# Optimization experiments

Measured on AMD Instinct MI355X. Metric: run time of the kernel, lower is better.

## Reference

```python
import jax, jax.numpy as jnp
import numpy as np

MODEL_DIM = 128
N_ATOMS = 2048
ATOM_SIZE = 512
N_SAMPLES = 2 ** 15
FACTOR = 1.0
TAU = 1.0
B, E = 8, 64


def _stack(x, w0, b0, w1, b1, w2, b2):
    # LinearOutputStack(model_dim, 2, out_channels=...): 2 hidden layers + output
    h = jax.nn.leaky_relu(x @ w0 + b0, 0.2)
    h = jax.nn.leaky_relu(h @ w1 + b1, 0.2)
    return h @ w2 + b2


def _fft_shift(a, shift):
    # a: [B, E, n], shift: [B, E, 1] (fractional shift in units of n samples * 0.5)
    n = a.shape[-1]
    shift_samples = shift * n * 0.5  # [B, E, 1]
    a = jnp.pad(a, ((0, 0), (0, 0), (0, n * 2)))
    spec = jnp.fft.rfft(a, axis=-1, norm='ortho')  # [B, E, n_coeffs] complex
    n_coeffs = spec.shape[-1]
    phase = (jnp.arange(n_coeffs) * 2j * jnp.pi) / n_coeffs  # [n_coeffs]
    spec = spec * jnp.exp(-phase[None, None, :] * shift_samples)
    samples = jnp.fft.irfft(spec, axis=-1, norm='ortho')
    return samples[..., :n]


def setup_inputs() -> dict:
    key = jax.random.key(0)
    ks = jax.random.split(key, 24)
    w = lambda k, i, o: (jax.random.normal(k, (i, o), jnp.float32) * 0.1)
    z = lambda o: jnp.zeros((o,), jnp.float32)
    return {
        'x': jax.random.normal(ks[0], (B, E, MODEL_DIM), jnp.float32),
        'times': jax.random.uniform(ks[1], (B, E, 1), jnp.float32),
        'gumbel_u': jax.random.uniform(ks[2], (B, E, N_ATOMS), jnp.float32),
        'atoms': jax.random.uniform(ks[3], (N_ATOMS, ATOM_SIZE), jnp.float32, -1.0, 1.0),
        'tw0': w(ks[4], MODEL_DIM, MODEL_DIM), 'tb0': z(MODEL_DIM),
        'tw1': w(ks[5], MODEL_DIM, MODEL_DIM), 'tb1': z(MODEL_DIM),
        'tw2': w(ks[6], MODEL_DIM, 1), 'tb2': z(1),
        'sw0': w(ks[7], MODEL_DIM, MODEL_DIM), 'sb0': z(MODEL_DIM),
        'sw1': w(ks[8], MODEL_DIM, MODEL_DIM), 'sb1': z(MODEL_DIM),
        'sw2': w(ks[9], MODEL_DIM, N_ATOMS), 'sb2': z(N_ATOMS),
        'aw0': w(ks[10], MODEL_DIM, MODEL_DIM), 'ab0': z(MODEL_DIM),
        'aw1': w(ks[11], MODEL_DIM, MODEL_DIM), 'ab1': z(MODEL_DIM),
        'aw2': w(ks[12], MODEL_DIM, 1), 'ab2': z(1),
    }


def reference(x, times, gumbel_u, atoms,
              tw0, tb0, tw1, tb1, tw2, tb2,
              sw0, sb0, sw1, sb1, sw2, sb2,
              aw0, ab0, aw1, ab1, aw2, ab2):
    time = jax.nn.sigmoid(_stack(x, tw0, tb0, tw1, tb1, tw2, tb2)) * FACTOR + times  # [B,E,1]
    amp = _stack(x, aw0, ab0, aw1, ab1, aw2, ab2) ** 2  # [B,E,1]
    logits = _stack(x, sw0, sb0, sw1, sb1, sw2, sb2)  # [B,E,N_ATOMS]

    # hard gumbel-softmax with straight-through estimator
    eps = 1e-10
    g = -jnp.log(-jnp.log(gumbel_u + eps) + eps)
    y_soft = jax.nn.softmax((logits + g) / TAU, axis=-1)
    y_hard = jax.nn.one_hot(jnp.argmax(y_soft, axis=-1), N_ATOMS, dtype=y_soft.dtype)
    sel = y_hard - jax.lax.stop_gradient(y_soft) + y_soft

    normed = atoms / (jnp.linalg.norm(atoms, axis=-1, keepdims=True) + 1e-8)
    a = (sel @ normed) * amp  # [B,E,ATOM_SIZE]
    a = jnp.pad(a, ((0, 0), (0, 0), (0, N_SAMPLES - ATOM_SIZE)))  # [B,E,N_SAMPLES]
    final = _fft_shift(a, time)
    return jnp.sum(final, axis=1, keepdims=True)  # [B,1,N_SAMPLES]
```

## Files before the change

kernel.cpp:

```cpp
#include <hip/hip_runtime.h>
#include <math.h>

#define MD 128
#define NA 2048
#define AS 512
#define NS 32768
#define NBE 512
#define W1 768
#define W2 1280
#define PI 3.14159265358979323846
#define KTH ((float)(PI / 98304.0))

__device__ __forceinline__ float lrelu(float v) { return v > 0.f ? v : 0.2f * v; }

__device__ __forceinline__ float p8_far(float tf, float4 A, float4 B, float4 C)
{
  float u  = tf - A.x;
  float th = u * KTH;
  float sn = __sinf(th);
  float cs = __cosf(th);
  float c  = cs * __builtin_amdgcn_rcpf(sn);
  float u2  = __builtin_fmaf(c, c, 1.f);
  float c2  = c + c;
  float u22 = u2 + u2;
  float a2  = c * u2;
  float a3  = (-1.f / 3.f) * __builtin_fmaf(c2, a2, u2 * u2);
  float a4  = 0.5f * __builtin_fmaf(-c, a3, u2 * a2);
  float s5  = __builtin_fmaf(c2, a4, a2 * a2);
  s5        = __builtin_fmaf(-u22, a3, s5);
  float a5  = -0.2f * s5;
  float s6  = __builtin_fmaf(c, a5, a2 * a3);
  s6        = __builtin_fmaf(-u2, a4, s6);
  float a6  = (-1.f / 3.f) * s6;
  float s7  = __builtin_fmaf(c2, a6, a3 * a3);
  s7        = __builtin_fmaf(-u22, a5, s7);
  s7        = __builtin_fmaf(2.f * a2, a4, s7);
  float a7  = (-1.f / 7.f) * s7;
  float s8  = __builtin_fmaf(c, a7, a3 * a4);
  s8        = __builtin_fmaf(-u2, a6, s8);
  s8        = __builtin_fmaf(a2, a5, s8);
  float a8  = -0.25f * s8;
  float y = c * A.w;
  y = __builtin_fmaf(-u2, B.x, y);
  y = __builtin_fmaf(a2, B.y, y);
  y = __builtin_fmaf(a3, B.z, y);
  y = __builtin_fmaf(a4, B.w, y);
  y = __builtin_fmaf(a5, C.x, y);
  y = __builtin_fmaf(a6, C.y, y);
  y = __builtin_fmaf(a7, C.z, y);
  y = __builtin_fmaf(a8, C.w, y);
  bool farq = (tf < A.y) || (tf >= A.z);
  return farq ? y : 0.f;
}

__global__ __launch_bounds__(128) void hidden_kernel(
    const float* __restrict__ x, const float* __restrict__ times,
    const float* __restrict__ tw0, const float* __restrict__ tb0,
    const float* __restrict__ tw1, const float* __restrict__ tb1,
    const float* __restrict__ tw2, const float* __restrict__ tb2,
    const float* __restrict__ sw0, const float* __restrict__ sb0,
    const float* __restrict__ sw1, const float* __restrict__ sb1,
    const float* __restrict__ aw0, const float* __restrict__ ab0,
    const float* __restrict__ aw1, const float* __restrict__ ab1,
    const float* __restrict__ aw2, const float* __restrict__ ab2,
    float* __restrict__ timev, float* __restrict__ ampv,
    float* __restrict__ h2sel, float* __restrict__ out)
{
  const int rg = blockIdx.x;
  const int stack = blockIdx.y;
  const int tid = threadIdx.x;

  {
    const int gtid = (stack * 256 + rg) * 128 + tid;
    if (gtid < (8 * NS) / 4)
      ((float4*)out)[gtid] = make_float4(0.f, 0.f, 0.f, 0.f);
  }

  __shared__ float xs[2][MD];
  __shared__ double dA[2][MD], dB[2][MD];
  __shared__ float fA[2][MD], fB[2][MD];

#pragma unroll
  for (int j = 0; j < 2; ++j) xs[j][tid] = x[(rg * 2 + j) * MD + tid];
  __syncthreads();

  if (stack == 0) {
    {
      double b = (double)tb0[tid];
      double s[2] = {b, b};
#pragma unroll 8
      for (int k = 0; k < MD; ++k) {
        double w = (double)tw0[k * MD + tid];
#pragma unroll
        for (int j = 0; j < 2; ++j) s[j] += (double)xs[j][k] * w;
      }
#pragma unroll
      for (int j = 0; j < 2; ++j) dA[j][tid] = s[j] > 0.0 ? s[j] : 0.2 * s[j];
      __syncthreads();
    }
    {
      double b = (double)tb1[tid];
      double s[2] = {b, b};
#pragma unroll 8
      for (int k = 0; k < MD; ++k) {
        double w = (double)tw1[k * MD + tid];
#pragma unroll
        for (int j = 0; j < 2; ++j) s[j] += dA[j][k] * w;
      }
#pragma unroll
      for (int j = 0; j < 2; ++j) dB[j][tid] = s[j] > 0.0 ? s[j] : 0.2 * s[j];
      __syncthreads();
    }
    {
      double w2 = (double)tw2[tid];
#pragma unroll
      for (int j = 0; j < 2; ++j) dA[j][tid] = dB[j][tid] * w2;
      __syncthreads();
      for (int off = 64; off > 0; off >>= 1) {
        if (tid < off) {
#pragma unroll
          for (int j = 0; j < 2; ++j) dA[j][tid] += dA[j][tid + off];
        }
        __syncthreads();
      }
      if (tid == 0) {
#pragma unroll
        for (int j = 0; j < 2; ++j) {
          double tval = dA[j][0] + (double)tb2[0];
          double sg = 1.0 / (1.0 + exp(-tval));
          float tf = (float)sg;
          timev[rg * 2 + j] = tf * 1.0f + times[rg * 2 + j];
        }
      }
    }
  } else if (stack == 1) {
    {
      float b = ab0[tid];
      float s[2] = {b, b};
#pragma unroll 8
      for (int k = 0; k < MD; ++k) {
        float w = aw0[k * MD + tid];
#pragma unroll
        for (int j = 0; j < 2; ++j) s[j] += xs[j][k] * w;
      }
#pragma unroll
      for (int j = 0; j < 2; ++j) fA[j][tid] = lrelu(s[j]);
      __syncthreads();
    }
    {
      float b = ab1[tid];
      float s[2] = {b, b};
#pragma unroll 8
      for (int k = 0; k < MD; ++k) {
        float w = aw1[k * MD + tid];
#pragma unroll
        for (int j = 0; j < 2; ++j) s[j] += fA[j][k] * w;
      }
#pragma unroll
      for (int j = 0; j < 2; ++j) fB[j][tid] = lrelu(s[j]);
      __syncthreads();
    }
    {
      float w2 = aw2[tid];
#pragma unroll
      for (int j = 0; j < 2; ++j) fA[j][tid] = fB[j][tid] * w2;
      __syncthreads();
      for (int off = 64; off > 0; off >>= 1) {
        if (tid < off) {
#pragma unroll
          for (int j = 0; j < 2; ++j) fA[j][tid] += fA[j][tid + off];
        }
        __syncthreads();
      }
      if (tid == 0) {
#pragma unroll
        for (int j = 0; j < 2; ++j) {
          float av = fA[j][0] + ab2[0];
          ampv[rg * 2 + j] = av * av;
        }
      }
    }
  } else {
    {
      float b = sb0[tid];
      float s[2] = {b, b};
#pragma unroll 8
      for (int k = 0; k < MD; ++k) {
        float w = sw0[k * MD + tid];
#pragma unroll
        for (int j = 0; j < 2; ++j) s[j] += xs[j][k] * w;
      }
#pragma unroll
      for (int j = 0; j < 2; ++j) fA[j][tid] = lrelu(s[j]);
      __syncthreads();
    }
    {
      float b = sb1[tid];
      float s[2] = {b, b};
#pragma unroll 8
      for (int k = 0; k < MD; ++k) {
        float w = sw1[k * MD + tid];
#pragma unroll
        for (int j = 0; j < 2; ++j) s[j] += fA[j][k] * w;
      }
#pragma unroll
      for (int j = 0; j < 2; ++j)
        h2sel[(rg * 2 + j) * MD + tid] = lrelu(s[j]);
    }
  }
}

__global__ __launch_bounds__(128) void logits_kernel(
    const float* __restrict__ h2sel, const float* __restrict__ gu,
    const float* __restrict__ sw2, const float* __restrict__ sb2,
    float2* __restrict__ partials)
{
  const int ot = blockIdx.x;
  const int beg = blockIdx.y;
  const int tid = threadIdx.x;
  const int o = ot * 128 + tid;
  const int wave = tid >> 6, lane = tid & 63;

  __shared__ float h2s[4][MD];
  __shared__ float wv[2][4];
  __shared__ int wi[2][4];

#pragma unroll
  for (int j = 0; j < 4; ++j) h2s[j][tid] = h2sel[(beg * 4 + j) * MD + tid];
  __syncthreads();

  float b = sb2[o];
  float acc[4] = {b, b, b, b};
#pragma unroll 16
  for (int k = 0; k < MD; ++k) {
    float w = sw2[k * NA + o];
#pragma unroll
    for (int j = 0; j < 4; ++j) acc[j] = fmaf(h2s[j][k], w, acc[j]);
  }

#pragma unroll
  for (int j = 0; j < 4; ++j) {
    float u = gu[(beg * 4 + j) * NA + o];
    float g = -__logf(-__logf(u + 1e-10f) + 1e-10f);
    float v = acc[j] + g;
    int idx = o;
    for (int off = 32; off > 0; off >>= 1) {
      float ov = __shfl_xor(v, off);
      int oi = __shfl_xor(idx, off);
      if (ov > v || (ov == v && oi < idx)) { v = ov; idx = oi; }
    }
    if (lane == 0) { wv[wave][j] = v; wi[wave][j] = idx; }
  }
  __syncthreads();
  if (tid == 0) {
#pragma unroll
    for (int j = 0; j < 4; ++j) {
      float v0 = wv[0][j], v1 = wv[1][j];
      int i0 = wi[0][j], i1 = wi[1][j];
      bool take1 = (v1 > v0) || (v1 == v0 && i1 < i0);
      float bv = take1 ? v1 : v0;
      int bi = take1 ? i1 : i0;
      partials[(beg * 4 + j) * 16 + ot] = make_float2(bv, __int_as_float(bi));
    }
  }
}

__global__ __launch_bounds__(128) void finalize_kernel(
    const float2* __restrict__ partials, const float* __restrict__ timev,
    const float* __restrict__ ampv, const float* __restrict__ atoms,
    float* __restrict__ G, int* __restrict__ m0s, float* __restrict__ fracs,
    float4* __restrict__ params, float4* __restrict__ mom2)
{
  const int be = blockIdx.x;
  const int tid = threadIdx.x;
  __shared__ float red[128];
  __shared__ float m_red[128][13];
  __shared__ float sc_coef, sc_inv;
  __shared__ int sc_idx;

  if (tid < 64) {
    float v = -3.4e38f;
    int idx = 0x7fffffff;
    if (tid < 16) {
      float2 p = partials[be * 16 + tid];
      v = p.x;
      idx = __float_as_int(p.y);
    }
    for (int off = 8; off > 0; off >>= 1) {
      float ov = __shfl_xor(v, off);
      int oi = __shfl_xor(idx, off);
      if (ov > v || (ov == v && oi < idx)) { v = ov; idx = oi; }
    }
    if (tid == 0) sc_idx = idx;
  }
  __syncthreads();
  const int idx = sc_idx;

  const float4 a4 = ((const float4*)(atoms + (size_t)idx * AS))[tid];

  {
    float ss = a4.x * a4.x + a4.y * a4.y + a4.z * a4.z + a4.w * a4.w;
    red[tid] = ss;
    __syncthreads();
    for (int off = 64; off > 0; off >>= 1) {
      if (tid < off) red[tid] += red[tid + off];
      __syncthreads();
    }
    if (tid == 0) {
      sc_inv = 1.f / (sqrtf(red[0]) + 1e-8f);
      double Nc = (double)timev[be] * (1610612736.0 / 49153.0);
      double rr = rint(Nc);
      int m0 = (int)rr;
      float fr = (float)(Nc - rr);
      if (fabsf(fr) < 1e-9f) fr = (fr < 0.f) ? -1e-9f : 1e-9f;
      m0s[be] = m0;
      fracs[be] = fr;
      sc_coef = ampv[be] * ((m0 & 1) ? 1.0f : -1.0f) *
                sinf((float)PI * fr) * (1.0f / 98304.0f);
      red[64] = (float)m0;
      red[65] = fr;
    }
    __syncthreads();
  }

  const float cf = sc_coef * sc_inv;
  float mk[13];
#pragma unroll
  for (int k = 0; k < 13; ++k) mk[k] = 0.f;
  const float av4[4] = {a4.x * cf, a4.y * cf, a4.z * cf, a4.w * cf};
  float4 gv4;
  float* gvp = (float*)&gv4;
  const int t0 = tid * 4;
#pragma unroll
  for (int j = 0; j < 4; ++j) {
    const int t = t0 + j;
    float gv = (j & 1) ? -av4[j] : av4[j];
    gvp[j] = gv;
    float q = (255.5f - (float)t) * KTH;
    float pw = gv;
    mk[0] += pw;
#pragma unroll
    for (int k = 1; k < 13; ++k) { pw *= q; mk[k] += pw; }
  }
  ((float4*)(G + (size_t)be * AS))[tid] = gv4;
#pragma unroll
  for (int k = 0; k < 13; ++k) m_red[tid][k] = mk[k];
  __syncthreads();
  for (int off = 64; off > 0; off >>= 1) {
    if (tid < off) {
#pragma unroll
      for (int k = 0; k < 13; ++k) m_red[tid][k] += m_red[tid + off][k];
    }
    __syncthreads();
  }
  if (tid == 0) {
    int m0 = (int)red[64];
    float fr = red[65];
    float uc = (float)((double)m0 + (double)fr + 255.5);
    params[be * 3 + 0] = make_float4(uc, (float)(m0 - W1), (float)(m0 + W2), m_red[0][0]);
    params[be * 3 + 1] = make_float4(m_red[0][1], m_red[0][2], m_red[0][3], m_red[0][4]);
    params[be * 3 + 2] = make_float4(m_red[0][5], m_red[0][6], m_red[0][7], m_red[0][8]);
    mom2[be] = make_float4(m_red[0][9], m_red[0][10], m_red[0][11], m_red[0][12]);
  }
}

__global__ __launch_bounds__(256) void field_kernel(
    const float4* __restrict__ params, const float4* __restrict__ mom2,
    const float* __restrict__ G, const int* __restrict__ m0s,
    const float* __restrict__ fracs, float* __restrict__ out)
{
  __shared__ float4 SMEM[768];
  const int bid = blockIdx.x;
  const int tid = threadIdx.x;

  if (bid >= 512) {
    const int idx2 = bid - 512;
    const int b = idx2 >> 7;
    const int seg = idx2 & 127;
    float* Cf   = (float*)SMEM;
    int*   scnt = (int*)(Cf + 32);
    int*   slst = scnt + 2;

    const int w = tid >> 6;
    const int e = tid & 63;
    if (w < 2) {
      const int tile = 2 * seg + w;
      const int be = b * 64 + e;
      const float4 A  = params[be * 3 + 0];
      const float4 B4 = params[be * 3 + 1];
      const float4 C4 = params[be * 3 + 2];
      const float4 D4 = mom2[be];
      const float M[13] = {A.w, B4.x, B4.y, B4.z, B4.w,
                           C4.x, C4.y, C4.z, C4.w, D4.x, D4.y, D4.z, D4.w};

      const float ts = (float)(tile * 128);
      const float te = ts + 128.f;
      const float lo = A.y, hi = A.z;
      const bool inter   = (lo < te) && (hi > ts);
      const bool inside  = (lo <= ts) && (te <= hi);
      const bool special = inter && !inside;

      float Bj[13];
#pragma unroll
      for (int j = 0; j < 13; ++j) Bj[j] = 0.f;

      if (!inter) {
        const float th = (ts + 63.5f - A.x) * KTH;
        const float sn = __sinf(th), cs = __cosf(th);
        const float c = cs * __builtin_amdgcn_rcpf(sn);
        float a[13];
        a[0] = c; a[1] = -__builtin_fmaf(c, c, 1.f);
        float s;
        s = 2.f * a[0] * a[1];                                      a[2]  = -0.5f * s;
        s = __builtin_fmaf(2.f * a[0], a[2], a[1] * a[1]);          a[3]  = (-1.f / 3.f) * s;
        s = 2.f * (a[0] * a[3] + a[1] * a[2]);                      a[4]  = -0.25f * s;
        s = __builtin_fmaf(2.f, a[0] * a[4] + a[1] * a[3], a[2] * a[2]); a[5] = -0.2f * s;
        s = 2.f * (a[0] * a[5] + a[1] * a[4] + a[2] * a[3]);        a[6]  = (-1.f / 6.f) * s;
        s = __builtin_fmaf(2.f, a[0] * a[6] + a[1] * a[5] + a[2] * a[4], a[3] * a[3]); a[7] = (-1.f / 7.f) * s;
        s = 2.f * (a[0] * a[7] + a[1] * a[6] + a[2] * a[5] + a[3] * a[4]); a[8] = -0.125f * s;
        s = __builtin_fmaf(2.f, a[0] * a[8] + a[1] * a[7] + a[2] * a[6] + a[3] * a[5], a[4] * a[4]); a[9] = (-1.f / 9.f) * s;
        s = 2.f * (a[0] * a[9] + a[1] * a[8] + a[2] * a[7] + a[3] * a[6] + a[4] * a[5]); a[10] = -0.1f * s;
        s = __builtin_fmaf(2.f, a[0] * a[10] + a[1] * a[9] + a[2] * a[8] + a[3] * a[7] + a[4] * a[6], a[5] * a[5]); a[11] = (-1.f / 11.f) * s;
        s = 2.f * (a[0] * a[11] + a[1] * a[10] + a[2] * a[9] + a[3] * a[8] + a[4] * a[7] + a[5] * a[6]); a[12] = (-1.f / 12.f) * s;

        const float BIN[13][13] = {
          {1,0,0,0,0,0,0,0,0,0,0,0,0},
          {1,1,0,0,0,0,0,0,0,0,0,0,0},
          {1,2,1,0,0,0,0,0,0,0,0,0,0},
          {1,3,3,1,0,0,0,0,0,0,0,0,0},
          {1,4,6,4,1,0,0,0,0,0,0,0,0},
          {1,5,10,10,5,1,0,0,0,0,0,0,0},
          {1,6,15,20,15,6,1,0,0,0,0,0,0},
          {1,7,21,35,35,21,7,1,0,0,0,0,0},
          {1,8,28,56,70,56,28,8,1,0,0,0,0},
          {1,9,36,84,126,126,84,36,9,1,0,0,0},
          {1,10,45,120,210,252,210,120,45,10,1,0,0},
          {1,11,55,165,330,462,462,330,165,55,11,1,0},
          {1,12,66,220,495,792,924,792,495,220,66,12,1}};
#pragma unroll
        for (int j = 0; j < 13; ++j) {
          float acc = 0.f;
#pragma unroll
          for (int m = j; m < 13; ++m)
            acc = __builtin_fmaf(BIN[m][j] * a[m], M[m - j], acc);
          Bj[j] = acc;
        }
      }

#pragma unroll
      for (int j = 0; j < 13; ++j) {
#pragma unroll
        for (int off = 32; off > 0; off >>= 1)
          Bj[j] += __shfl_xor(Bj[j], off);
      }
      if (e == 0) {
#pragma unroll
        for (int j = 0; j < 13; ++j) Cf[w * 16 + j] = Bj[j];
      }
      unsigned long long msk = __ballot(special);
      if (special) {
        int pos = __popcll(msk & ((1ull << e) - 1ull));
        slst[w * 64 + pos] = be;
      }
      if (e == 0) scnt[w] = (int)__popcll(msk);
    }
    __syncthreads();

    const int t = seg * 256 + tid;
    const int tw = tid >> 7;
    const float* cc = Cf + tw * 16;
    const float tf = (float)t;
    const float h = (tf - ((float)((2 * seg + tw) * 128) + 63.5f)) * KTH;
    float y = cc[12];
    y = __builtin_fmaf(y, h, cc[11]);
    y = __builtin_fmaf(y, h, cc[10]);
    y = __builtin_fmaf(y, h, cc[9]);
    y = __builtin_fmaf(y, h, cc[8]);
    y = __builtin_fmaf(y, h, cc[7]);
    y = __builtin_fmaf(y, h, cc[6]);
    y = __builtin_fmaf(y, h, cc[5]);
    y = __builtin_fmaf(y, h, cc[4]);
    y = __builtin_fmaf(y, h, cc[3]);
    y = __builtin_fmaf(y, h, cc[2]);
    y = __builtin_fmaf(y, h, cc[1]);
    y = __builtin_fmaf(y, h, cc[0]);

    const int cnt = scnt[tw];
    for (int i = 0; i < cnt; ++i) {
      const int se = slst[tw * 64 + i];
      const float4 A  = params[se * 3 + 0];
      const float4 B4 = params[se * 3 + 1];
      const float4 C4 = params[se * 3 + 2];
      y += p8_far(tf, A, B4, C4);
    }
    atomicAdd(&out[b * NS + t], (t & 1) ? -y : y);
    return;
  }

  const int be = bid;
  const int m0 = m0s[be];
  const int start = m0 - W1;
  if (start >= NS) return;
  const float fr = fracs[be];
  const int b = be >> 6;

  float4* Tsplit = SMEM;
  float*  Tf = (float*)Tsplit;
  float*  Gl = (float*)(SMEM + 640);
  const float4* Gl4 = SMEM + 640;

  for (int i = tid; i < AS; i += 256) Gl[i] = G[be * AS + i];
  for (int i = tid; i < 2560; i += 256) {
    int v = start - 511 + i;
    float w = (float)(v - m0) - fr;
    float th = w * KTH;
    float q = th * th;
    float sn = th * __builtin_fmaf(q, __builtin_fmaf(q, (1.f / 120.f), (-1.f / 6.f)), 1.f);
    float cs = __builtin_fmaf(q, __builtin_fmaf(q, (1.f / 24.f), -0.5f), 1.f);
    float val = cs * __builtin_amdgcn_rcpf(sn);
    int g = i >> 2;
    int s = (g >> 1) * 4 + (i & 3) + (g & 1) * 1280;
    Tf[s] = val;
  }
  __syncthreads();

  float acc[8];
#pragma unroll
  for (int r = 0; r < 8; ++r) acc[r] = 0.f;

  float Wf[16];
  {
    float4 qa = Tsplit[tid];
    float4 qb = Tsplit[320 + tid];
    Wf[0] = qa.x; Wf[1] = qa.y; Wf[2] = qa.z; Wf[3] = qa.w;
    Wf[4] = qb.x; Wf[5] = qb.y; Wf[6] = qb.z; Wf[7] = qb.w;
  }
#pragma unroll 4
  for (int k = 0; k < 64; ++k) {
    float4 qa = Tsplit[tid + k + 1];
    float4 qb = Tsplit[320 + tid + k + 1];
    Wf[8]  = qa.x; Wf[9]  = qa.y; Wf[10] = qa.z; Wf[11] = qa.w;
    Wf[12] = qb.x; Wf[13] = qb.y; Wf[14] = qb.z; Wf[15] = qb.w;
    const int tc = 504 - 8 * k;
    const float4 gq0 = Gl4[tc >> 2];
    const float4 gq1 = Gl4[(tc >> 2) + 1];
    const float gvals[8] = {gq0.x, gq0.y, gq0.z, gq0.w,
                            gq1.x, gq1.y, gq1.z, gq1.w};
#pragma unroll
    for (int d = 0; d < 8; ++d) {
      const float gv = gvals[d];
#pragma unroll
      for (int r = 0; r < 8; ++r)
        acc[r] = fmaf(gv, Wf[7 + r - d], acc[r]);
    }
#pragma unroll
    for (int m = 0; m < 8; ++m) Wf[m] = Wf[m + 8];
  }

  const int tb = start + tid * 8;
#pragma unroll
  for (int r = 0; r < 8; ++r) {
    int t = tb + r;
    if (t >= 0 && t < NS) {
      float v = (t & 1) ? -acc[r] : acc[r];
      atomicAdd(&out[b * NS + t], v);
    }
  }
}

extern "C" void kernel_launch(void* const* d_in, const int* in_sizes, int n_in,
                              void* d_out, int out_size, void* d_ws, size_t ws_size,
                              hipStream_t stream) {
  const float* x     = (const float*)d_in[0];
  const float* times = (const float*)d_in[1];
  const float* gu    = (const float*)d_in[2];
  const float* atoms = (const float*)d_in[3];
  const float* tw0 = (const float*)d_in[4];  const float* tb0 = (const float*)d_in[5];
  const float* tw1 = (const float*)d_in[6];  const float* tb1 = (const float*)d_in[7];
  const float* tw2 = (const float*)d_in[8];  const float* tb2 = (const float*)d_in[9];
  const float* sw0 = (const float*)d_in[10]; const float* sb0 = (const float*)d_in[11];
  const float* sw1 = (const float*)d_in[12]; const float* sb1 = (const float*)d_in[13];
  const float* sw2 = (const float*)d_in[14]; const float* sb2 = (const float*)d_in[15];
  const float* aw0 = (const float*)d_in[16]; const float* ab0 = (const float*)d_in[17];
  const float* aw1 = (const float*)d_in[18]; const float* ab1 = (const float*)d_in[19];
  const float* aw2 = (const float*)d_in[20]; const float* ab2 = (const float*)d_in[21];

  char* wsb = (char*)d_ws;
  float*  G        = (float*)wsb;
  int*    m0s      = (int*)(wsb + 1048576);
  float*  fracs    = (float*)(wsb + 1050624);
  float4* params   = (float4*)(wsb + 1052672);
  float*  timev    = (float*)(wsb + 1077248);
  float*  ampv     = (float*)(wsb + 1079296);
  float4* mom2     = (float4*)(wsb + 1081344);
  float*  h2sel    = (float*)(wsb + 1089536);
  float2* partials = (float2*)(wsb + 1351680);

  hidden_kernel<<<dim3(NBE / 2, 3), 128, 0, stream>>>(
      x, times, tw0, tb0, tw1, tb1, tw2, tb2,
      sw0, sb0, sw1, sb1, aw0, ab0, aw1, ab1, aw2, ab2,
      timev, ampv, h2sel, (float*)d_out);

  logits_kernel<<<dim3(16, NBE / 4), 128, 0, stream>>>(h2sel, gu, sw2, sb2, partials);

  finalize_kernel<<<NBE, 128, 0, stream>>>(partials, timev, ampv, atoms,
                                           G, m0s, fracs, params, mom2);

  field_kernel<<<1536, 256, 0, stream>>>(params, mom2, G, m0s, fracs,
                                         (float*)d_out);
}
```

Baseline: 67.03 us.

## Fuse finalize into logits via last-block ticket and stage MLP weights in LDS

The finalize kernel is merged into the logits kernel. Each block atomically increments a per-group counter, and the last of the 16 blocks for a group of four rows performs the argmax reduction, atom normalization and moment computation. This removes one kernel launch and its dependency gap. The hidden MLP layers also load weight tiles of 32 rows into shared memory with float4 copies instead of reading strided global values per k. The ticket counters are reset inside hidden_kernel, and the fused path adds serial per-group tail work in a few blocks plus extra barriers.

```diff
diff --git a/kernel.cpp b/kernel.cpp
--- a/kernel.cpp
+++ b/kernel.cpp
@@ -64,7 +64,8 @@
     const float* __restrict__ aw1, const float* __restrict__ ab1,
     const float* __restrict__ aw2, const float* __restrict__ ab2,
     float* __restrict__ timev, float* __restrict__ ampv,
-    float* __restrict__ h2sel, float* __restrict__ out)
+    float* __restrict__ h2sel, int* __restrict__ ready,
+    float* __restrict__ out)
 {
   const int rg = blockIdx.x;
   const int stack = blockIdx.y;
@@ -74,8 +75,10 @@
     const int gtid = (stack * 256 + rg) * 128 + tid;
     if (gtid < (8 * NS) / 4)
       ((float4*)out)[gtid] = make_float4(0.f, 0.f, 0.f, 0.f);
-  }
-
+    if (blockIdx.x == 0 && blockIdx.y == 0) ready[tid] = 0;
+  }
+
+  __shared__ float wS[32 * MD];
   __shared__ float xs[2][MD];
   __shared__ double dA[2][MD], dB[2][MD];
   __shared__ float fA[2][MD], fB[2][MD];
@@ -88,24 +91,37 @@
     {
       double b = (double)tb0[tid];
       double s[2] = {b, b};
+      for (int kc = 0; kc < MD; kc += 32) {
+        __syncthreads();
+#pragma unroll
+        for (int i = 0; i < 8; ++i)
+          ((float4*)wS)[tid + i * 128] = ((const float4*)(tw0 + kc * MD))[tid + i * 128];
+        __syncthreads();
 #pragma unroll 8
-      for (int k = 0; k < MD; ++k) {
-        double w = (double)tw0[k * MD + tid];
-#pragma unroll
-        for (int j = 0; j < 2; ++j) s[j] += (double)xs[j][k] * w;
+        for (int k2 = 0; k2 < 32; ++k2) {
+          double w = (double)wS[k2 * MD + tid];
+          s[0] += (double)xs[0][kc + k2] * w;
+          s[1] += (double)xs[1][kc + k2] * w;
+        }
       }
 #pragma unroll
       for (int j = 0; j < 2; ++j) dA[j][tid] = s[j] > 0.0 ? s[j] : 0.2 * s[j];
-      __syncthreads();
     }
     {
       double b = (double)tb1[tid];
       double s[2] = {b, b};
+      for (int kc = 0; kc < MD; kc += 32) {
+        __syncthreads();
+#pragma unroll
+        for (int i = 0; i < 8; ++i)
+          ((float4*)wS)[tid + i * 128] = ((const float4*)(tw1 + kc * MD))[tid + i * 128];
+        __syncthreads();
 #pragma unroll 8
-      for (int k = 0; k < MD; ++k) {
-        double w = (double)tw1[k * MD + tid];
-#pragma unroll
-        for (int j = 0; j < 2; ++j) s[j] += dA[j][k] * w;
+        for (int k2 = 0; k2 < 32; ++k2) {
+          double w = (double)wS[k2 * MD + tid];
+          s[0] += dA[0][kc + k2] * w;
+          s[1] += dA[1][kc + k2] * w;
+        }
       }
 #pragma unroll
       for (int j = 0; j < 2; ++j) dB[j][tid] = s[j] > 0.0 ? s[j] : 0.2 * s[j];
@@ -137,24 +153,37 @@
     {
       float b = ab0[tid];
       float s[2] = {b, b};
+      for (int kc = 0; kc < MD; kc += 32) {
+        __syncthreads();
+#pragma unroll
+        for (int i = 0; i < 8; ++i)
+          ((float4*)wS)[tid + i * 128] = ((const float4*)(aw0 + kc * MD))[tid + i * 128];
+        __syncthreads();
 #pragma unroll 8
-      for (int k = 0; k < MD; ++k) {
-        float w = aw0[k * MD + tid];
-#pragma unroll
-        for (int j = 0; j < 2; ++j) s[j] += xs[j][k] * w;
+        for (int k2 = 0; k2 < 32; ++k2) {
+          float w = wS[k2 * MD + tid];
+          s[0] = fmaf(xs[0][kc + k2], w, s[0]);
+          s[1] = fmaf(xs[1][kc + k2], w, s[1]);
+        }
       }
 #pragma unroll
       for (int j = 0; j < 2; ++j) fA[j][tid] = lrelu(s[j]);
-      __syncthreads();
     }
     {
       float b = ab1[tid];
       float s[2] = {b, b};
+      for (int kc = 0; kc < MD; kc += 32) {
+        __syncthreads();
+#pragma unroll
+        for (int i = 0; i < 8; ++i)
+          ((float4*)wS)[tid + i * 128] = ((const float4*)(aw1 + kc * MD))[tid + i * 128];
+        __syncthreads();
 #pragma unroll 8
-      for (int k = 0; k < MD; ++k) {
-        float w = aw1[k * MD + tid];
-#pragma unroll
-        for (int j = 0; j < 2; ++j) s[j] += fA[j][k] * w;
+        for (int k2 = 0; k2 < 32; ++k2) {
+          float w = wS[k2 * MD + tid];
+          s[0] = fmaf(fA[0][kc + k2], w, s[0]);
+          s[1] = fmaf(fA[1][kc + k2], w, s[1]);
+        }
       }
 #pragma unroll
       for (int j = 0; j < 2; ++j) fB[j][tid] = lrelu(s[j]);
@@ -184,24 +213,37 @@
     {
       float b = sb0[tid];
       float s[2] = {b, b};
+      for (int kc = 0; kc < MD; kc += 32) {
+        __syncthreads();
+#pragma unroll
+        for (int i = 0; i < 8; ++i)
+          ((float4*)wS)[tid + i * 128] = ((const float4*)(sw0 + kc * MD))[tid + i * 128];
+        __syncthreads();
 #pragma unroll 8
-      for (int k = 0; k < MD; ++k) {
-        float w = sw0[k * MD + tid];
-#pragma unroll
-        for (int j = 0; j < 2; ++j) s[j] += xs[j][k] * w;
+        for (int k2 = 0; k2 < 32; ++k2) {
+          float w = wS[k2 * MD + tid];
+          s[0] = fmaf(xs[0][kc + k2], w, s[0]);
+          s[1] = fmaf(xs[1][kc + k2], w, s[1]);
+        }
       }
 #pragma unroll
       for (int j = 0; j < 2; ++j) fA[j][tid] = lrelu(s[j]);
-      __syncthreads();
     }
     {
       float b = sb1[tid];
       float s[2] = {b, b};
+      for (int kc = 0; kc < MD; kc += 32) {
+        __syncthreads();
+#pragma unroll
+        for (int i = 0; i < 8; ++i)
+          ((float4*)wS)[tid + i * 128] = ((const float4*)(sw1 + kc * MD))[tid + i * 128];
+        __syncthreads();
 #pragma unroll 8
-      for (int k = 0; k < MD; ++k) {
-        float w = sw1[k * MD + tid];
-#pragma unroll
-        for (int j = 0; j < 2; ++j) s[j] += fA[j][k] * w;
+        for (int k2 = 0; k2 < 32; ++k2) {
+          float w = wS[k2 * MD + tid];
+          s[0] = fmaf(fA[0][kc + k2], w, s[0]);
+          s[1] = fmaf(fA[1][kc + k2], w, s[1]);
+        }
       }
 #pragma unroll
       for (int j = 0; j < 2; ++j)
@@ -210,10 +252,14 @@
   }
 }
 
-__global__ __launch_bounds__(128) void logits_kernel(
+__global__ __launch_bounds__(128) void logits_fin_kernel(
     const float* __restrict__ h2sel, const float* __restrict__ gu,
     const float* __restrict__ sw2, const float* __restrict__ sb2,
-    float2* __restrict__ partials)
+    const float* __restrict__ timev, const float* __restrict__ ampv,
+    const float* __restrict__ atoms,
+    float2* __restrict__ partials, int* __restrict__ ready,
+    float* __restrict__ G, int* __restrict__ m0s, float* __restrict__ fracs,
+    float4* __restrict__ params, float4* __restrict__ mom2)
 {
   const int ot = blockIdx.x;
   const int beg = blockIdx.y;
@@ -224,6 +270,11 @@
   __shared__ float h2s[4][MD];
   __shared__ float wv[2][4];
   __shared__ int wi[2][4];
+  __shared__ int sh_ticket;
+  __shared__ float red[128];
+  __shared__ float m_red[128][13];
+  __shared__ float sc_coef, sc_inv;
+  __shared__ int sc_idx;
 
 #pragma unroll
   for (int j = 0; j < 4; ++j) h2s[j][tid] = h2sel[(beg * 4 + j) * MD + tid];
@@ -262,105 +313,101 @@
       int bi = take1 ? i1 : i0;
       partials[(beg * 4 + j) * 16 + ot] = make_float2(bv, __int_as_float(bi));
     }
-  }
-}
-
-__global__ __launch_bounds__(128) void finalize_kernel(
-    const float2* __restrict__ partials, const float* __restrict__ timev,
-    const float* __restrict__ ampv, const float* __restrict__ atoms,
-    float* __restrict__ G, int* __restrict__ m0s, float* __restrict__ fracs,
-    float4* __restrict__ params, float4* __restrict__ mom2)
-{
-  const int be = blockIdx.x;
-  const int tid = threadIdx.x;
-  __shared__ float red[128];
-  __shared__ float m_red[128][13];
-  __shared__ float sc_coef, sc_inv;
-  __shared__ int sc_idx;
-
-  if (tid < 64) {
-    float v = -3.4e38f;
-    int idx = 0x7fffffff;
-    if (tid < 16) {
-      float2 p = partials[be * 16 + tid];
-      v = p.x;
-      idx = __float_as_int(p.y);
-    }
-    for (int off = 8; off > 0; off >>= 1) {
-      float ov = __shfl_xor(v, off);
-      int oi = __shfl_xor(idx, off);
-      if (ov > v || (ov == v && oi < idx)) { v = ov; idx = oi; }
-    }
-    if (tid == 0) sc_idx = idx;
+    __threadfence();
+    sh_ticket = atomicAdd(&ready[beg], 1);
   }
   __syncthreads();
-  const int idx = sc_idx;
-
-  const float4 a4 = ((const float4*)(atoms + (size_t)idx * AS))[tid];
-
-  {
-    float ss = a4.x * a4.x + a4.y * a4.y + a4.z * a4.z + a4.w * a4.w;
-    red[tid] = ss;
+  if (sh_ticket != 15) return;
+
+  __threadfence();
+  for (int jj = 0; jj < 4; ++jj) {
+    const int be = beg * 4 + jj;
+    __syncthreads();
+
+    if (tid < 64) {
+      float v = -3.4e38f;
+      int idx = 0x7fffffff;
+      if (tid < 16) {
+        volatile float* pp = (volatile float*)(partials + be * 16 + tid);
+        v = pp[0];
+        idx = __float_as_int(pp[1]);
+      }
+      for (int off = 8; off > 0; off >>= 1) {
+        float ov = __shfl_xor(v, off);
+        int oi = __shfl_xor(idx, off);
+        if (ov > v || (ov == v && oi < idx)) { v = ov; idx = oi; }
+      }
+      if (tid == 0) sc_idx = idx;
+    }
+    __syncthreads();
+    const int idx = sc_idx;
+
+    const float4 a4 = ((const float4*)(atoms + (size_t)idx * AS))[tid];
+
+    {
+      float ss = a4.x * a4.x + a4.y * a4.y + a4.z * a4.z + a4.w * a4.w;
+      red[tid] = ss;
+      __syncthreads();
+      for (int off = 64; off > 0; off >>= 1) {
+        if (tid < off) red[tid] += red[tid + off];
+        __syncthreads();
+      }
+      if (tid == 0) {
+        sc_inv = 1.f / (sqrtf(red[0]) + 1e-8f);
+        double Nc = (double)timev[be] * (1610612736.0 / 49153.0);
+        double rr = rint(Nc);
+        int m0 = (int)rr;
+        float fr = (float)(Nc - rr);
+        if (fabsf(fr) < 1e-9f) fr = (fr < 0.f) ? -1e-9f : 1e-9f;
+        m0s[be] = m0;
+        fracs[be] = fr;
+        sc_coef = ampv[be] * ((m0 & 1) ? 1.0f : -1.0f) *
+                  sinf((float)PI * fr) * (1.0f / 98304.0f);
+        red[64] = (float)m0;
+        red[65] = fr;
+      }
+      __syncthreads();
+    }
+
+    const float cf = sc_coef * sc_inv;
+    float mk[13];
+#pragma unroll
+    for (int k = 0; k < 13; ++k) mk[k] = 0.f;
+    const float av4[4] = {a4.x * cf, a4.y * cf, a4.z * cf, a4.w * cf};
+    float4 gv4;
+    float* gvp = (float*)&gv4;
+    const int t0 = tid * 4;
+#pragma unroll
+    for (int j = 0; j < 4; ++j) {
+      const int t = t0 + j;
+      float gv = (j & 1) ? -av4[j] : av4[j];
+      gvp[j] = gv;
+      float q = (255.5f - (float)t) * KTH;
+      float pw = gv;
+      mk[0] += pw;
+#pragma unroll
+      for (int k = 1; k < 13; ++k) { pw *= q; mk[k] += pw; }
+    }
+    ((float4*)(G + (size_t)be * AS))[tid] = gv4;
+#pragma unroll
+    for (int k = 0; k < 13; ++k) m_red[tid][k] = mk[k];
     __syncthreads();
     for (int off = 64; off > 0; off >>= 1) {
-      if (tid < off) red[tid] += red[tid + off];
+      if (tid < off) {
+#pragma unroll
+        for (int k = 0; k < 13; ++k) m_red[tid][k] += m_red[tid + off][k];
+      }
       __syncthreads();
     }
     if (tid == 0) {
-      sc_inv = 1.f / (sqrtf(red[0]) + 1e-8f);
-      double Nc = (double)timev[be] * (1610612736.0 / 49153.0);
-      double rr = rint(Nc);
-      int m0 = (int)rr;
-      float fr = (float)(Nc - rr);
-      if (fabsf(fr) < 1e-9f) fr = (fr < 0.f) ? -1e-9f : 1e-9f;
-      m0s[be] = m0;
-      fracs[be] = fr;
-      sc_coef = ampv[be] * ((m0 & 1) ? 1.0f : -1.0f) *
-                sinf((float)PI * fr) * (1.0f / 98304.0f);
-      red[64] = (float)m0;
-      red[65] = fr;
-    }
-    __syncthreads();
-  }
-
-  const float cf = sc_coef * sc_inv;
-  float mk[13];
-#pragma unroll
-  for (int k = 0; k < 13; ++k) mk[k] = 0.f;
-  const float av4[4] = {a4.x * cf, a4.y * cf, a4.z * cf, a4.w * cf};
-  float4 gv4;
-  float* gvp = (float*)&gv4;
-  const int t0 = tid * 4;
-#pragma unroll
-  for (int j = 0; j < 4; ++j) {
-    const int t = t0 + j;
-    float gv = (j & 1) ? -av4[j] : av4[j];
-    gvp[j] = gv;
-    float q = (255.5f - (float)t) * KTH;
-    float pw = gv;
-    mk[0] += pw;
-#pragma unroll
-    for (int k = 1; k < 13; ++k) { pw *= q; mk[k] += pw; }
-  }
-  ((float4*)(G + (size_t)be * AS))[tid] = gv4;
-#pragma unroll
-  for (int k = 0; k < 13; ++k) m_red[tid][k] = mk[k];
-  __syncthreads();
-  for (int off = 64; off > 0; off >>= 1) {
-    if (tid < off) {
-#pragma unroll
-      for (int k = 0; k < 13; ++k) m_red[tid][k] += m_red[tid + off][k];
-    }
-    __syncthreads();
-  }
-  if (tid == 0) {
-    int m0 = (int)red[64];
-    float fr = red[65];
-    float uc = (float)((double)m0 + (double)fr + 255.5);
-    params[be * 3 + 0] = make_float4(uc, (float)(m0 - W1), (float)(m0 + W2), m_red[0][0]);
-    params[be * 3 + 1] = make_float4(m_red[0][1], m_red[0][2], m_red[0][3], m_red[0][4]);
-    params[be * 3 + 2] = make_float4(m_red[0][5], m_red[0][6], m_red[0][7], m_red[0][8]);
-    mom2[be] = make_float4(m_red[0][9], m_red[0][10], m_red[0][11], m_red[0][12]);
+      int m0 = (int)red[64];
+      float fr = red[65];
+      float uc = (float)((double)m0 + (double)fr + 255.5);
+      params[be * 3 + 0] = make_float4(uc, (float)(m0 - W1), (float)(m0 + W2), m_red[0][0]);
+      params[be * 3 + 1] = make_float4(m_red[0][1], m_red[0][2], m_red[0][3], m_red[0][4]);
+      params[be * 3 + 2] = make_float4(m_red[0][5], m_red[0][6], m_red[0][7], m_red[0][8]);
+      mom2[be] = make_float4(m_red[0][9], m_red[0][10], m_red[0][11], m_red[0][12]);
+    }
   }
 }
 
@@ -595,16 +642,16 @@
   float4* mom2     = (float4*)(wsb + 1081344);
   float*  h2sel    = (float*)(wsb + 1089536);
   float2* partials = (float2*)(wsb + 1351680);
+  int*    ready    = (int*)(wsb + 1417216);
 
   hidden_kernel<<<dim3(NBE / 2, 3), 128, 0, stream>>>(
       x, times, tw0, tb0, tw1, tb1, tw2, tb2,
       sw0, sb0, sw1, sb1, aw0, ab0, aw1, ab1, aw2, ab2,
-      timev, ampv, h2sel, (float*)d_out);
-
-  logits_kernel<<<dim3(16, NBE / 4), 128, 0, stream>>>(h2sel, gu, sw2, sb2, partials);
-
-  finalize_kernel<<<NBE, 128, 0, stream>>>(partials, timev, ampv, atoms,
-                                           G, m0s, fracs, params, mom2);
+      timev, ampv, h2sel, ready, (float*)d_out);
+
+  logits_fin_kernel<<<dim3(16, NBE / 4), 128, 0, stream>>>(
+      h2sel, gu, sw2, sb2, timev, ampv, atoms,
+      partials, ready, G, m0s, fracs, params, mom2);
 
   field_kernel<<<1536, 256, 0, stream>>>(params, mom2, G, m0s, fracs,
                                          (float*)d_out);
```

New measurement: 125.1 us. +86.6%, slower.
